# Kernel tuning notes

Hardware: AMD Instinct MI355X
Metric: run time of the kernel (lower is better)

The kernel has to match this reference:

```python
import jax, jax.numpy as jnp
import numpy as np

B, T, D, H, A, BIAS_DIM, E = 8, 1024, 1024, 16, 64, 32, 262144  # A = attention_dim_per_head


def setup_inputs() -> dict:
    key = jax.random.key(0)
    ks = jax.random.split(key, 10)
    states = jax.random.normal(ks[0], (B, T, D), dtype=jnp.float32)
    key_states = jax.random.normal(ks[1], (B, T, D), dtype=jnp.float32)
    masks = (jax.random.uniform(ks[2], (B, T, T)) < 0.1).astype(jnp.float32)
    # sparse bias edges: columns (edge_type, batch, query_idx, key_idx)
    et = jax.random.randint(ks[3], (E, 1), 0, BIAS_DIM)
    bi = jax.random.randint(ks[4], (E, 1), 0, B)
    qi = jax.random.randint(ks[5], (E, 1), 0, T)
    ki = jax.random.randint(ks[6], (E, 1), 0, T)
    attention_bias = jnp.concatenate([et, bi, qi, ki], axis=1).astype(jnp.int64)
    # parameters (xavier-like scale)
    def xav(k, shape, fan_in, fan_out):
        a = np.sqrt(6.0 / (fan_in + fan_out))
        return jax.random.uniform(k, shape, minval=-a, maxval=a, dtype=jnp.float32)
    Wq = xav(ks[7], (D, H, A), D, H * A)
    Wk = xav(jax.random.fold_in(ks[7], 1), (D, H, A), D, H * A)
    Wv = xav(jax.random.fold_in(ks[7], 2), (D, H, A), D, H * A)
    Wout = xav(ks[8], (H, A, D), H * A, D)
    bias_embs = xav(ks[9], (BIAS_DIM, A), BIAS_DIM, A)
    bias_scalar = xav(jax.random.fold_in(ks[9], 1), (A, 1), A, 1)
    return {"states": states, "key_states": key_states, "masks": masks,
            "attention_bias": attention_bias, "Wq": Wq, "Wk": Wk, "Wv": Wv,
            "Wout": Wout, "bias_embs": bias_embs, "bias_scalar": bias_scalar}


def reference(states, key_states, masks, attention_bias, Wq, Wk, Wv, Wout, bias_embs, bias_scalar):
    q = jnp.einsum('btd,dha->btha', states, Wq)
    k = jnp.einsum('btd,dha->btha', key_states, Wk)
    v = jnp.einsum('btd,dha->btha', key_states, Wv)
    alpha = jnp.einsum('bkha,bqha->bhqk', k, q)  # [B,H,Q,K]
    # sparse edge bias: embed edge types, project to scalar, scatter into [B,Q,K]
    bvals = (bias_embs[attention_bias[:, 0]] @ bias_scalar)[:, 0]  # [E]
    Bq, Hh, Q, K = alpha.shape
    bs = jnp.zeros((Bq, Q, K), dtype=alpha.dtype).at[
        attention_bias[:, 1], attention_bias[:, 2], attention_bias[:, 3]].set(bvals)
    ksum = k.sum(-1)  # [B,K,H]
    alpha = alpha + jnp.einsum('bqk,bkh->bhqk', bs, ksum)
    alpha = alpha * (1.0 / jnp.sqrt(jnp.float32(A)))
    alpha = alpha - masks[:, None, :, :] * jnp.finfo(jnp.float32).max
    alpha = jax.nn.softmax(alpha, axis=-1)
    context = jnp.einsum('bhqk,bkha->bqha', alpha, v)
    return jnp.einsum('btha,had->btd', context, Wout)
```

## Files before the change

### kernel.cpp

```cpp
#include <hip/hip_runtime.h>
#include <hip/hip_bf16.h>

#define BB 8
#define TT 1024
#define DD 1024
#define HH 16
#define AA 64
#define EE 262144

typedef unsigned short u16;
typedef unsigned int u32;
typedef short bf16x8 __attribute__((ext_vector_type(8)));
typedef float f32x4 __attribute__((ext_vector_type(4)));

__device__ __forceinline__ float bf2f(u16 u) {
    union { float f; u32 i; } c; c.i = ((u32)u) << 16; return c.f;
}
__device__ __forceinline__ u16 f2bf(float f) {
    union { float f; u32 i; } c; c.f = f;
    u32 x = c.i;
    return (u16)((x + 0x7FFFu + ((x >> 16) & 1u)) >> 16);
}
__device__ __forceinline__ u32 pack2bf(float a, float b) {
    union { __hip_bfloat162 h; u32 u; } c;
    c.h = __float22bfloat162_rn(float2{a, b});
    return c.u;
}

#define GLDS16(gp, lp)                                                        \
    __builtin_amdgcn_global_load_lds(                                         \
        (const __attribute__((address_space(1))) u32*)(const void*)(gp),      \
        (__attribute__((address_space(3))) u32*)(void*)(lp), 16, 0, 0)

#define MFMA(a, b, c) __builtin_amdgcn_mfma_f32_16x16x32_bf16((a), (b), (c), 0, 0, 0)

__global__ __launch_bounds__(256) void cvt(const float* __restrict__ src,
                                           u16* __restrict__ dst) {
    size_t i = ((size_t)blockIdx.x * 256 + threadIdx.x) * 8;
    f32x4 a = *(const f32x4*)(src + i);
    f32x4 b = *(const f32x4*)(src + i + 4);
    u32 o[4];
    o[0] = pack2bf(a[0], a[1]);
    o[1] = pack2bf(a[2], a[3]);
    o[2] = pack2bf(b[0], b[1]);
    o[3] = pack2bf(b[2], b[3]);
    *(bf16x8*)(dst + i) = *(bf16x8*)o;
}

__global__ __launch_bounds__(256) void mbinit(const float* __restrict__ masks,
                                              float* __restrict__ mb) {
    size_t i = ((size_t)blockIdx.x * 256 + threadIdx.x) * 8;
    f32x4 a = *(const f32x4*)(masks + i);
    f32x4 b = *(const f32x4*)(masks + i + 4);
    f32x4 oa, ob;
#pragma unroll
    for (int j = 0; j < 4; j++) {
        oa[j] = (a[j] != 0.f) ? -1.0e30f : 0.f;
        ob[j] = (b[j] != 0.f) ? -1.0e30f : 0.f;
    }
    *(f32x4*)(mb + i) = oa;
    *(f32x4*)(mb + i + 4) = ob;
}

__global__ __launch_bounds__(256) void scat_max(const int* __restrict__ ab,
                                                int* __restrict__ idx) {
    int e = blockIdx.x * 256 + threadIdx.x;
    const int* rec = ab + (size_t)e * 4;
    int b = rec[1], q = rec[2], k = rec[3];
    atomicMax(&idx[((((size_t)b << 10) + q) << 10) + k], e);
}

__global__ __launch_bounds__(256) void scat_res(const int* __restrict__ ab,
                                                const int* __restrict__ idx,
                                                const float* __restrict__ be,
                                                const float* __restrict__ bsc,
                                                float* __restrict__ mb) {
    __shared__ float proj[32];
    int tid = threadIdx.x;
    if (tid < 32) {
        float s = 0.f;
        for (int a = 0; a < 64; a++) s += be[tid * 64 + a] * bsc[a];
        proj[tid] = s * 0.125f;
    }
    __syncthreads();
    int e = blockIdx.x * 256 + tid;
    const int* rec = ab + (size_t)e * 4;
    int et = rec[0], b = rec[1], q = rec[2], k = rec[3];
    size_t cell = ((((size_t)b << 10) + q) << 10) + k;
    if (idx[cell] == e && mb[cell] > -1.0e29f) mb[cell] = proj[et];
}

__global__ __launch_bounds__(256) void tr_w(const float* __restrict__ s0,
                                            const float* __restrict__ s1,
                                            const float* __restrict__ s2,
                                            const float* __restrict__ s3,
                                            u16* __restrict__ dstbase) {
    __shared__ u16 t[64 * 72];
    int tid = threadIdx.x;
    int z = blockIdx.z;
    const float* src = (z == 0) ? s0 : (z == 1) ? s1 : (z == 2) ? s2 : s3;
    u16* dst = dstbase + (size_t)z * 1024 * 1024;
    int row0 = blockIdx.y * 64, col0 = blockIdx.x * 64;
    int r = tid >> 2, c0 = (tid & 3) * 16;
    const float* sp = src + (size_t)(row0 + r) * 1024 + col0 + c0;
    f32x4 f0 = *(const f32x4*)(sp);
    f32x4 f1 = *(const f32x4*)(sp + 4);
    f32x4 f2_ = *(const f32x4*)(sp + 8);
    f32x4 f3 = *(const f32x4*)(sp + 12);
#pragma unroll
    for (int j = 0; j < 4; j++) {
        t[r * 72 + c0 + j] = f2bf(f0[j]);
        t[r * 72 + c0 + 4 + j] = f2bf(f1[j]);
        t[r * 72 + c0 + 8 + j] = f2bf(f2_[j]);
        t[r * 72 + c0 + 12 + j] = f2bf(f3[j]);
    }
    __syncthreads();
    bf16x8 o0, o1;
#pragma unroll
    for (int j = 0; j < 8; j++) o0[j] = (short)t[(c0 + j) * 72 + r];
#pragma unroll
    for (int j = 0; j < 8; j++) o1[j] = (short)t[(c0 + 8 + j) * 72 + r];
    *(bf16x8*)(dst + (size_t)(col0 + r) * 1024 + row0 + c0) = o0;
    *(bf16x8*)(dst + (size_t)(col0 + r) * 1024 + row0 + c0 + 8) = o1;
}

__global__ __launch_bounds__(256) void gemm3(const u16* __restrict__ A,
                                             const u16* __restrict__ BT,
                                             void* __restrict__ C,
                                             int mode, float scale) {
    __shared__ u16 Asm[128 * 32];
    __shared__ u16 Bsm[128 * 32];
    int tid = threadIdx.x;
    int wave = tid >> 6, lane = tid & 63;
    int quad = lane >> 4, l16 = lane & 15;
    int wm = wave >> 1, wn = wave & 1;
    int mbase = blockIdx.y * 128, nbase = blockIdx.x * 128;
    f32x4 acc[4][4] = {};
    int srow = wave * 32 + (lane >> 2);
    int scol = (lane & 3) * 8;
    const u16* gA = A + (size_t)(mbase + srow) * 1024 + scol;
    const u16* gB = BT + (size_t)(nbase + srow) * 1024 + scol;
    u16* lA = Asm + wave * 32 * 32;
    u16* lB = Bsm + wave * 32 * 32;
    for (int k0 = 0; k0 < 1024; k0 += 32) {
        __syncthreads();
        GLDS16(gA + k0, lA);
        GLDS16(gA + k0 + 16 * 1024, lA + 16 * 32);
        GLDS16(gB + k0, lB);
        GLDS16(gB + k0 + 16 * 1024, lB + 16 * 32);
        __syncthreads();
        bf16x8 af[4], bfr[4];
#pragma unroll
        for (int mt = 0; mt < 4; mt++)
            af[mt] = *(const bf16x8*)&Asm[(wm * 64 + mt * 16 + l16) * 32 + quad * 8];
#pragma unroll
        for (int nt = 0; nt < 4; nt++)
            bfr[nt] = *(const bf16x8*)&Bsm[(wn * 64 + nt * 16 + l16) * 32 + quad * 8];
#pragma unroll
        for (int mt = 0; mt < 4; mt++)
#pragma unroll
            for (int nt = 0; nt < 4; nt++)
                acc[mt][nt] = MFMA(af[mt], bfr[nt], acc[mt][nt]);
    }
#pragma unroll
    for (int mt = 0; mt < 4; mt++)
#pragma unroll
        for (int nt = 0; nt < 4; nt++)
#pragma unroll
            for (int r = 0; r < 4; r++) {
                int gm = mbase + wm * 64 + mt * 16 + quad * 4 + r;
                int gn = nbase + wn * 64 + nt * 16 + l16;
                if (mode == 0) {
                    ((float*)C)[(size_t)gm * 1024 + gn] = acc[mt][nt][r];
                } else {
                    int b = gm >> 10, t = gm & 1023, h = gn >> 6, a = gn & 63;
                    ((u16*)C)[(((size_t)(b * 16 + h) * 1024) + t) * 64 + a] =
                        f2bf(acc[mt][nt][r] * scale);
                }
            }
}

__global__ __launch_bounds__(256) void tr_v(const u16* __restrict__ v,
                                            u16* __restrict__ vT) {
    __shared__ u16 t[64 * 72];
    int tid = threadIdx.x;
    int bh = blockIdx.y;
    int t0 = blockIdx.x * 64;
    int r = tid >> 2, c0 = (tid & 3) * 16;
    const u16* src = v + (size_t)bh * 1024 * 64;
    u16* dst = vT + (size_t)bh * 64 * 1024;
    bf16x8 v0 = *(const bf16x8*)(src + (size_t)(t0 + r) * 64 + c0);
    bf16x8 v1 = *(const bf16x8*)(src + (size_t)(t0 + r) * 64 + c0 + 8);
    *(bf16x8*)&t[r * 72 + c0] = v0;
    *(bf16x8*)&t[r * 72 + c0 + 8] = v1;
    __syncthreads();
    bf16x8 o0, o1;
#pragma unroll
    for (int j = 0; j < 8; j++) o0[j] = (short)t[(c0 + j) * 72 + r];
#pragma unroll
    for (int j = 0; j < 8; j++) o1[j] = (short)t[(c0 + 8 + j) * 72 + r];
    *(bf16x8*)(dst + (size_t)r * 1024 + t0 + c0) = o0;
    *(bf16x8*)(dst + (size_t)r * 1024 + t0 + c0 + 8) = o1;
}

__global__ __launch_bounds__(256) void ksumk(const u16* __restrict__ k,
                                             float* __restrict__ ks) {
    int i = blockIdx.x * 256 + threadIdx.x;
    const u16* kp = k + (size_t)i * 64;
    float s = 0.f;
#pragma unroll
    for (int c = 0; c < 64; c += 8) {
        bf16x8 v = *(const bf16x8*)(kp + c);
#pragma unroll
        for (int j = 0; j < 8; j++) s += bf2f((u16)v[j]);
    }
    ks[i] = s;
}

__global__ __launch_bounds__(256) void attn2(const u16* __restrict__ qbuf,
                                             const u16* __restrict__ kbuf,
                                             const u16* __restrict__ vT,
                                             const float* __restrict__ ksum,
                                             const float* __restrict__ mb,
                                             u16* __restrict__ ctx) {
    __shared__ u16 Ksm[64 * 72];
    __shared__ u16 Vsm[64 * 72];
    __shared__ u16 Psm[4 * 16 * 72];
    __shared__ float sksm[64];
    __shared__ float lsm[64];
    int tid = threadIdx.x;
    int wave = tid >> 6, lane = tid & 63;
    int quad = lane >> 4, l16 = lane & 15;
    int qb = blockIdx.x, h = blockIdx.y, b = blockIdx.z;
    int bh = b * 16 + h;
    const u16* qp = qbuf + (size_t)bh * 65536;
    const u16* kp = kbuf + (size_t)bh * 65536;
    const u16* vp = vT + (size_t)bh * 65536;
    const float* ksp = ksum + (size_t)bh * 1024;
    int q0 = qb * 64 + wave * 16;
    const float* mbp = mb + ((size_t)b * 1024 + (q0 + l16)) * 1024;

    bf16x8 qf0 = *(const bf16x8*)(qp + (size_t)(q0 + l16) * 64 + quad * 8);
    bf16x8 qf1 = *(const bf16x8*)(qp + (size_t)(q0 + l16) * 64 + 32 + quad * 8);

    f32x4 oacc[4] = {};
    float lsum = 0.f;
    int srow = tid >> 2, sc0 = (tid & 3) * 16;
    u16* pw = &Psm[wave * 16 * 72];

    for (int kb = 0; kb < 1024; kb += 64) {
        bf16x8 k0 = *(const bf16x8*)(kp + (size_t)(kb + srow) * 64 + sc0);
        bf16x8 k1 = *(const bf16x8*)(kp + (size_t)(kb + srow) * 64 + sc0 + 8);
        bf16x8 v0 = *(const bf16x8*)(vp + (size_t)srow * 1024 + kb + sc0);
        bf16x8 v1 = *(const bf16x8*)(vp + (size_t)srow * 1024 + kb + sc0 + 8);
        f32x4 mbv[4];
#pragma unroll
        for (int nt = 0; nt < 4; nt++)
            mbv[nt] = *(const f32x4*)(mbp + kb + nt * 16 + quad * 4);
        __syncthreads();
        *(bf16x8*)&Ksm[srow * 72 + sc0] = k0;
        *(bf16x8*)&Ksm[srow * 72 + sc0 + 8] = k1;
        *(bf16x8*)&Vsm[srow * 72 + sc0] = v0;
        *(bf16x8*)&Vsm[srow * 72 + sc0 + 8] = v1;
        if (tid < 64) sksm[tid] = ksp[kb + tid];
        __syncthreads();

        f32x4 sacc[4];
#pragma unroll
        for (int nt = 0; nt < 4; nt++) sacc[nt] = f32x4{-20.f, -20.f, -20.f, -20.f};
#pragma unroll
        for (int nt = 0; nt < 4; nt++) {
            bf16x8 kf0 = *(const bf16x8*)&Ksm[(nt * 16 + l16) * 72 + quad * 8];
            bf16x8 kf1 = *(const bf16x8*)&Ksm[(nt * 16 + l16) * 72 + 32 + quad * 8];
            sacc[nt] = MFMA(kf0, qf0, sacc[nt]);
            sacc[nt] = MFMA(kf1, qf1, sacc[nt]);
        }

#pragma unroll
        for (int nt = 0; nt < 4; nt++) {
            f32x4 k4 = *(const f32x4*)&sksm[nt * 16 + quad * 4];
            float p[4];
#pragma unroll
            for (int r = 0; r < 4; r++) {
                float e = __expf(sacc[nt][r] + mbv[nt][r] * k4[r]);
                p[r] = (mbv[nt][r] > -1.0e29f) ? e : 0.f;
                lsum += p[r];
            }
            *(u32*)&pw[l16 * 72 + nt * 16 + quad * 4] = pack2bf(p[0], p[1]);
            *(u32*)&pw[l16 * 72 + nt * 16 + quad * 4 + 2] = pack2bf(p[2], p[3]);
        }

#pragma unroll
        for (int s = 0; s < 2; s++) {
            bf16x8 pf = *(const bf16x8*)&pw[l16 * 72 + s * 32 + quad * 8];
#pragma unroll
            for (int at = 0; at < 4; at++) {
                bf16x8 vf = *(const bf16x8*)&Vsm[(at * 16 + l16) * 72 + s * 32 + quad * 8];
                oacc[at] = MFMA(pf, vf, oacc[at]);
            }
        }
    }

    lsum += __shfl_xor(lsum, 16);
    lsum += __shfl_xor(lsum, 32);
    if (lane < 16) lsm[wave * 16 + lane] = lsum;
    __syncthreads();

#pragma unroll
    for (int r = 0; r < 4; r++) {
        float linv = 1.0f / lsm[wave * 16 + quad * 4 + r];
        int q = q0 + quad * 4 + r;
#pragma unroll
        for (int at = 0; at < 4; at++) {
            ctx[(((size_t)b * 1024 + q) * 16 + h) * 64 + at * 16 + l16] =
                f2bf(oacc[at][r] * linv);
        }
    }
}

extern "C" void kernel_launch(void* const* d_in, const int* in_sizes, int n_in,
                              void* d_out, int out_size, void* d_ws, size_t ws_size,
                              hipStream_t stream) {
    const float* states = (const float*)d_in[0];
    const float* key_states = (const float*)d_in[1];
    const float* masks = (const float*)d_in[2];
    const int* abias = (const int*)d_in[3];
    const float* Wq = (const float*)d_in[4];
    const float* Wk = (const float*)d_in[5];
    const float* Wv = (const float*)d_in[6];
    const float* Wout = (const float*)d_in[7];
    const float* be = (const float*)d_in[8];
    const float* bsc = (const float*)d_in[9];

    char* ws = (char*)d_ws;
    size_t off = 0;
    auto alloc = [&](size_t n) { void* p = ws + off; off += (n + 255) & ~(size_t)255; return p; };
    u16* wT = (u16*)alloc(4ull * 1024 * 1024 * 2);
    u16* sbf = (u16*)alloc((size_t)BB * TT * DD * 2);
    u16* kbf = (u16*)alloc((size_t)BB * TT * DD * 2);
    u16* qb_ = (u16*)alloc((size_t)BB * HH * TT * AA * 2);
    u16* kb_ = (u16*)alloc((size_t)BB * HH * TT * AA * 2);
    u16* vb_ = (u16*)alloc((size_t)BB * HH * TT * AA * 2);
    u16* vT_ = (u16*)alloc((size_t)BB * HH * AA * TT * 2);
    float* ks_ = (float*)alloc((size_t)BB * HH * TT * 4);
    float* mb_ = (float*)alloc((size_t)BB * TT * TT * 4);

    u16* wqT = wT;
    u16* wkT = wT + 1048576;
    u16* wvT = wT + 2097152;
    u16* woT = wT + 3145728;
    int* idx_ = (int*)qb_;
    u16* ctx_ = vb_;

    hipMemsetAsync(idx_, 0xFF, (size_t)BB * TT * TT * 4, stream);
    mbinit<<<dim3(4096), 256, 0, stream>>>(masks, mb_);
    scat_max<<<dim3(EE / 256), 256, 0, stream>>>(abias, idx_);
    scat_res<<<dim3(EE / 256), 256, 0, stream>>>(abias, idx_, be, bsc, mb_);
    tr_w<<<dim3(16, 16, 4), 256, 0, stream>>>(Wq, Wk, Wv, Wout, wT);
    cvt<<<dim3(4096), 256, 0, stream>>>(states, sbf);
    cvt<<<dim3(4096), 256, 0, stream>>>(key_states, kbf);
    gemm3<<<dim3(8, 64), 256, 0, stream>>>(sbf, wqT, qb_, 1, 0.125f);
    gemm3<<<dim3(8, 64), 256, 0, stream>>>(kbf, wkT, kb_, 1, 1.0f);
    gemm3<<<dim3(8, 64), 256, 0, stream>>>(kbf, wvT, vb_, 1, 1.0f);
    tr_v<<<dim3(16, 128), 256, 0, stream>>>(vb_, vT_);
    ksumk<<<dim3(512), 256, 0, stream>>>(kb_, ks_);
    attn2<<<dim3(16, 16, 8), 256, 0, stream>>>(qb_, kb_, vT_, ks_, mb_, ctx_);
    gemm3<<<dim3(8, 64), 256, 0, stream>>>(ctx_, woT, d_out, 0, 1.0f);
}
```

Before: 439.9 us.

## Store mask-bias in bf16, fuse K/V GEMMs, swizzle LDS, widen attention query tile

The dense mask/bias matrix is now stored as bf16 instead of fp32, halving its write and read traffic in the attention kernel. The projection GEMM uses K-tiles of 64 with an XOR-swizzled LDS layout, and the K and V projections run as one launch over a concatenated weight. The attention kernel processes 32 queries per wave, so each K/V tile in shared memory is reused twice as much. The risks are bf16 rounding of bias values and higher register pressure in attention.

```diff
diff --git a/kernel.cpp b/kernel.cpp
--- a/kernel.cpp
+++ b/kernel.cpp
@@ -10,6 +10,7 @@
 
 typedef unsigned short u16;
 typedef unsigned int u32;
+typedef short bf16x4 __attribute__((ext_vector_type(4)));
 typedef short bf16x8 __attribute__((ext_vector_type(8)));
 typedef float f32x4 __attribute__((ext_vector_type(4)));
 
@@ -48,18 +49,18 @@
 }
 
 __global__ __launch_bounds__(256) void mbinit(const float* __restrict__ masks,
-                                              float* __restrict__ mb) {
+                                              u16* __restrict__ mb) {
     size_t i = ((size_t)blockIdx.x * 256 + threadIdx.x) * 8;
     f32x4 a = *(const f32x4*)(masks + i);
     f32x4 b = *(const f32x4*)(masks + i + 4);
-    f32x4 oa, ob;
+    const u16 M = f2bf(-1.0e30f);
+    bf16x8 o;
 #pragma unroll
     for (int j = 0; j < 4; j++) {
-        oa[j] = (a[j] != 0.f) ? -1.0e30f : 0.f;
-        ob[j] = (b[j] != 0.f) ? -1.0e30f : 0.f;
-    }
-    *(f32x4*)(mb + i) = oa;
-    *(f32x4*)(mb + i + 4) = ob;
+        o[j] = (short)((a[j] != 0.f) ? M : 0);
+        o[4 + j] = (short)((b[j] != 0.f) ? M : 0);
+    }
+    *(bf16x8*)(mb + i) = o;
 }
 
 __global__ __launch_bounds__(256) void scat_max(const int* __restrict__ ab,
@@ -74,7 +75,7 @@
                                                 const int* __restrict__ idx,
                                                 const float* __restrict__ be,
                                                 const float* __restrict__ bsc,
-                                                float* __restrict__ mb) {
+                                                u16* __restrict__ mb) {
     __shared__ float proj[32];
     int tid = threadIdx.x;
     if (tid < 32) {
@@ -87,7 +88,7 @@
     const int* rec = ab + (size_t)e * 4;
     int et = rec[0], b = rec[1], q = rec[2], k = rec[3];
     size_t cell = ((((size_t)b << 10) + q) << 10) + k;
-    if (idx[cell] == e && mb[cell] > -1.0e29f) mb[cell] = proj[et];
+    if (idx[cell] == e && bf2f(mb[cell]) > -1.0e29f) mb[cell] = f2bf(proj[et]);
 }
 
 __global__ __launch_bounds__(256) void tr_w(const float* __restrict__ s0,
@@ -124,60 +125,81 @@
     *(bf16x8*)(dst + (size_t)(col0 + r) * 1024 + row0 + c0 + 8) = o1;
 }
 
-__global__ __launch_bounds__(256) void gemm3(const u16* __restrict__ A,
+__global__ __launch_bounds__(256) void gemm4(const u16* __restrict__ A,
                                              const u16* __restrict__ BT,
-                                             void* __restrict__ C,
-                                             int mode, float scale) {
-    __shared__ u16 Asm[128 * 32];
-    __shared__ u16 Bsm[128 * 32];
+                                             void* __restrict__ C0,
+                                             void* __restrict__ C1,
+                                             void* __restrict__ C2,
+                                             int mode, float sc0) {
+    __shared__ u16 Asm[128 * 64];
+    __shared__ u16 Bsm[128 * 64];
     int tid = threadIdx.x;
     int wave = tid >> 6, lane = tid & 63;
     int quad = lane >> 4, l16 = lane & 15;
     int wm = wave >> 1, wn = wave & 1;
     int mbase = blockIdx.y * 128, nbase = blockIdx.x * 128;
     f32x4 acc[4][4] = {};
-    int srow = wave * 32 + (lane >> 2);
-    int scol = (lane & 3) * 8;
-    const u16* gA = A + (size_t)(mbase + srow) * 1024 + scol;
-    const u16* gB = BT + (size_t)(nbase + srow) * 1024 + scol;
-    u16* lA = Asm + wave * 32 * 32;
-    u16* lB = Bsm + wave * 32 * 32;
-    for (int k0 = 0; k0 < 1024; k0 += 32) {
+    int srow = wave * 32 + (lane >> 3);
+    int schunk = (lane & 7) ^ (lane >> 3);
+    const u16* gA = A + (size_t)(mbase + srow) * 1024 + schunk * 8;
+    const u16* gB = BT + (size_t)(nbase + srow) * 1024 + schunk * 8;
+    u16* lA = Asm + wave * 2048;
+    u16* lB = Bsm + wave * 2048;
+    int sx = l16 & 7;
+    for (int k0 = 0; k0 < 1024; k0 += 64) {
         __syncthreads();
-        GLDS16(gA + k0, lA);
-        GLDS16(gA + k0 + 16 * 1024, lA + 16 * 32);
-        GLDS16(gB + k0, lB);
-        GLDS16(gB + k0 + 16 * 1024, lB + 16 * 32);
+#pragma unroll
+        for (int j = 0; j < 4; j++) GLDS16(gA + k0 + j * 8192, lA + j * 512);
+#pragma unroll
+        for (int j = 0; j < 4; j++) GLDS16(gB + k0 + j * 8192, lB + j * 512);
         __syncthreads();
-        bf16x8 af[4], bfr[4];
+#pragma unroll
+        for (int kk = 0; kk < 2; kk++) {
+            bf16x8 af[4], bfr[4];
+#pragma unroll
+            for (int mt = 0; mt < 4; mt++)
+                af[mt] = *(const bf16x8*)&Asm[(wm * 64 + mt * 16 + l16) * 64 +
+                                              ((kk * 4 + quad) ^ sx) * 8];
+#pragma unroll
+            for (int nt = 0; nt < 4; nt++)
+                bfr[nt] = *(const bf16x8*)&Bsm[(wn * 64 + nt * 16 + l16) * 64 +
+                                               ((kk * 4 + quad) ^ sx) * 8];
+#pragma unroll
+            for (int mt = 0; mt < 4; mt++)
+#pragma unroll
+                for (int nt = 0; nt < 4; nt++)
+                    acc[mt][nt] = MFMA(af[mt], bfr[nt], acc[mt][nt]);
+        }
+    }
+    if (mode == 0) {
 #pragma unroll
         for (int mt = 0; mt < 4; mt++)
-            af[mt] = *(const bf16x8*)&Asm[(wm * 64 + mt * 16 + l16) * 32 + quad * 8];
-#pragma unroll
-        for (int nt = 0; nt < 4; nt++)
-            bfr[nt] = *(const bf16x8*)&Bsm[(wn * 64 + nt * 16 + l16) * 32 + quad * 8];
+#pragma unroll
+            for (int nt = 0; nt < 4; nt++)
+#pragma unroll
+                for (int r = 0; r < 4; r++) {
+                    int gm = mbase + wm * 64 + mt * 16 + quad * 4 + r;
+                    int gn = nbase + wn * 64 + nt * 16 + l16;
+                    ((float*)C0)[(size_t)gm * 1024 + gn] = acc[mt][nt][r];
+                }
+    } else {
+        int mat = nbase >> 10;
+        int nloc = nbase & 1023;
+        u16* dst = (u16*)((mat == 0) ? C0 : (mat == 1) ? C1 : C2);
+        float sc = (mat == 0) ? sc0 : 1.0f;
 #pragma unroll
         for (int mt = 0; mt < 4; mt++)
 #pragma unroll
             for (int nt = 0; nt < 4; nt++)
-                acc[mt][nt] = MFMA(af[mt], bfr[nt], acc[mt][nt]);
-    }
-#pragma unroll
-    for (int mt = 0; mt < 4; mt++)
-#pragma unroll
-        for (int nt = 0; nt < 4; nt++)
-#pragma unroll
-            for (int r = 0; r < 4; r++) {
-                int gm = mbase + wm * 64 + mt * 16 + quad * 4 + r;
-                int gn = nbase + wn * 64 + nt * 16 + l16;
-                if (mode == 0) {
-                    ((float*)C)[(size_t)gm * 1024 + gn] = acc[mt][nt][r];
-                } else {
-                    int b = gm >> 10, t = gm & 1023, h = gn >> 6, a = gn & 63;
-                    ((u16*)C)[(((size_t)(b * 16 + h) * 1024) + t) * 64 + a] =
-                        f2bf(acc[mt][nt][r] * scale);
+#pragma unroll
+                for (int r = 0; r < 4; r++) {
+                    int gm = mbase + wm * 64 + mt * 16 + quad * 4 + r;
+                    int gnl = nloc + wn * 64 + nt * 16 + l16;
+                    int b = gm >> 10, t = gm & 1023, h = gnl >> 6, a = gnl & 63;
+                    dst[(((size_t)(b * 16 + h) * 1024) + t) * 64 + a] =
+                        f2bf(acc[mt][nt][r] * sc);
                 }
-            }
+    }
 }
 
 __global__ __launch_bounds__(256) void tr_v(const u16* __restrict__ v,
@@ -217,17 +239,17 @@
     ks[i] = s;
 }
 
-__global__ __launch_bounds__(256) void attn2(const u16* __restrict__ qbuf,
+__global__ __launch_bounds__(256) void attn3(const u16* __restrict__ qbuf,
                                              const u16* __restrict__ kbuf,
                                              const u16* __restrict__ vT,
                                              const float* __restrict__ ksum,
-                                             const float* __restrict__ mb,
+                                             const u16* __restrict__ mb,
                                              u16* __restrict__ ctx) {
     __shared__ u16 Ksm[64 * 72];
     __shared__ u16 Vsm[64 * 72];
     __shared__ u16 Psm[4 * 16 * 72];
     __shared__ float sksm[64];
-    __shared__ float lsm[64];
+    __shared__ float lsm[128];
     int tid = threadIdx.x;
     int wave = tid >> 6, lane = tid & 63;
     int quad = lane >> 4, l16 = lane & 15;
@@ -237,14 +259,19 @@
     const u16* kp = kbuf + (size_t)bh * 65536;
     const u16* vp = vT + (size_t)bh * 65536;
     const float* ksp = ksum + (size_t)bh * 1024;
-    int q0 = qb * 64 + wave * 16;
-    const float* mbp = mb + ((size_t)b * 1024 + (q0 + l16)) * 1024;
-
-    bf16x8 qf0 = *(const bf16x8*)(qp + (size_t)(q0 + l16) * 64 + quad * 8);
-    bf16x8 qf1 = *(const bf16x8*)(qp + (size_t)(q0 + l16) * 64 + 32 + quad * 8);
-
-    f32x4 oacc[4] = {};
-    float lsum = 0.f;
+    int q0w = qb * 128 + wave * 32;
+    const u16* mbp[2];
+    bf16x8 qf[2][2];
+#pragma unroll
+    for (int s = 0; s < 2; s++) {
+        int qs = q0w + s * 16;
+        mbp[s] = mb + ((size_t)b * 1024 + qs + l16) * 1024;
+        qf[s][0] = *(const bf16x8*)(qp + (size_t)(qs + l16) * 64 + quad * 8);
+        qf[s][1] = *(const bf16x8*)(qp + (size_t)(qs + l16) * 64 + 32 + quad * 8);
+    }
+
+    f32x4 oacc[2][4] = {};
+    float lsum[2] = {0.f, 0.f};
     int srow = tid >> 2, sc0 = (tid & 3) * 16;
     u16* pw = &Psm[wave * 16 * 72];
 
@@ -253,10 +280,12 @@
         bf16x8 k1 = *(const bf16x8*)(kp + (size_t)(kb + srow) * 64 + sc0 + 8);
         bf16x8 v0 = *(const bf16x8*)(vp + (size_t)srow * 1024 + kb + sc0);
         bf16x8 v1 = *(const bf16x8*)(vp + (size_t)srow * 1024 + kb + sc0 + 8);
-        f32x4 mbv[4];
-#pragma unroll
-        for (int nt = 0; nt < 4; nt++)
-            mbv[nt] = *(const f32x4*)(mbp + kb + nt * 16 + quad * 4);
+        bf16x4 mraw[2][4];
+#pragma unroll
+        for (int s = 0; s < 2; s++)
+#pragma unroll
+            for (int nt = 0; nt < 4; nt++)
+                mraw[s][nt] = *(const bf16x4*)(mbp[s] + kb + nt * 16 + quad * 4);
         __syncthreads();
         *(bf16x8*)&Ksm[srow * 72 + sc0] = k0;
         *(bf16x8*)&Ksm[srow * 72 + sc0 + 8] = k1;
@@ -265,57 +294,64 @@
         if (tid < 64) sksm[tid] = ksp[kb + tid];
         __syncthreads();
 
-        f32x4 sacc[4];
-#pragma unroll
-        for (int nt = 0; nt < 4; nt++) sacc[nt] = f32x4{-20.f, -20.f, -20.f, -20.f};
-#pragma unroll
-        for (int nt = 0; nt < 4; nt++) {
-            bf16x8 kf0 = *(const bf16x8*)&Ksm[(nt * 16 + l16) * 72 + quad * 8];
-            bf16x8 kf1 = *(const bf16x8*)&Ksm[(nt * 16 + l16) * 72 + 32 + quad * 8];
-            sacc[nt] = MFMA(kf0, qf0, sacc[nt]);
-            sacc[nt] = MFMA(kf1, qf1, sacc[nt]);
-        }
-
-#pragma unroll
-        for (int nt = 0; nt < 4; nt++) {
-            f32x4 k4 = *(const f32x4*)&sksm[nt * 16 + quad * 4];
-            float p[4];
-#pragma unroll
-            for (int r = 0; r < 4; r++) {
-                float e = __expf(sacc[nt][r] + mbv[nt][r] * k4[r]);
-                p[r] = (mbv[nt][r] > -1.0e29f) ? e : 0.f;
-                lsum += p[r];
+#pragma unroll
+        for (int s = 0; s < 2; s++) {
+            f32x4 sacc[4];
+#pragma unroll
+            for (int nt = 0; nt < 4; nt++) sacc[nt] = f32x4{-20.f, -20.f, -20.f, -20.f};
+#pragma unroll
+            for (int nt = 0; nt < 4; nt++) {
+                bf16x8 kf0 = *(const bf16x8*)&Ksm[(nt * 16 + l16) * 72 + quad * 8];
+                bf16x8 kf1 = *(const bf16x8*)&Ksm[(nt * 16 + l16) * 72 + 32 + quad * 8];
+                sacc[nt] = MFMA(kf0, qf[s][0], sacc[nt]);
+                sacc[nt] = MFMA(kf1, qf[s][1], sacc[nt]);
             }
-            *(u32*)&pw[l16 * 72 + nt * 16 + quad * 4] = pack2bf(p[0], p[1]);
-            *(u32*)&pw[l16 * 72 + nt * 16 + quad * 4 + 2] = pack2bf(p[2], p[3]);
-        }
-
-#pragma unroll
-        for (int s = 0; s < 2; s++) {
-            bf16x8 pf = *(const bf16x8*)&pw[l16 * 72 + s * 32 + quad * 8];
-#pragma unroll
-            for (int at = 0; at < 4; at++) {
-                bf16x8 vf = *(const bf16x8*)&Vsm[(at * 16 + l16) * 72 + s * 32 + quad * 8];
-                oacc[at] = MFMA(pf, vf, oacc[at]);
+#pragma unroll
+            for (int nt = 0; nt < 4; nt++) {
+                f32x4 k4 = *(const f32x4*)&sksm[nt * 16 + quad * 4];
+                float p[4];
+#pragma unroll
+                for (int r = 0; r < 4; r++) {
+                    float f = bf2f((u16)mraw[s][nt][r]);
+                    float e = __expf(sacc[nt][r] + f * k4[r]);
+                    p[r] = (f > -1.0e29f) ? e : 0.f;
+                    lsum[s] += p[r];
+                }
+                *(u32*)&pw[l16 * 72 + nt * 16 + quad * 4] = pack2bf(p[0], p[1]);
+                *(u32*)&pw[l16 * 72 + nt * 16 + quad * 4 + 2] = pack2bf(p[2], p[3]);
+            }
+#pragma unroll
+            for (int hs = 0; hs < 2; hs++) {
+                bf16x8 pf = *(const bf16x8*)&pw[l16 * 72 + hs * 32 + quad * 8];
+#pragma unroll
+                for (int at = 0; at < 4; at++) {
+                    bf16x8 vf = *(const bf16x8*)&Vsm[(at * 16 + l16) * 72 + hs * 32 + quad * 8];
+                    oacc[s][at] = MFMA(pf, vf, oacc[s][at]);
+                }
             }
         }
     }
 
-    lsum += __shfl_xor(lsum, 16);
-    lsum += __shfl_xor(lsum, 32);
-    if (lane < 16) lsm[wave * 16 + lane] = lsum;
+#pragma unroll
+    for (int s = 0; s < 2; s++) {
+        lsum[s] += __shfl_xor(lsum[s], 16);
+        lsum[s] += __shfl_xor(lsum[s], 32);
+        if (lane < 16) lsm[wave * 32 + s * 16 + lane] = lsum[s];
+    }
     __syncthreads();
 
 #pragma unroll
-    for (int r = 0; r < 4; r++) {
-        float linv = 1.0f / lsm[wave * 16 + quad * 4 + r];
-        int q = q0 + quad * 4 + r;
-#pragma unroll
-        for (int at = 0; at < 4; at++) {
-            ctx[(((size_t)b * 1024 + q) * 16 + h) * 64 + at * 16 + l16] =
-                f2bf(oacc[at][r] * linv);
+    for (int s = 0; s < 2; s++)
+#pragma unroll
+        for (int r = 0; r < 4; r++) {
+            float linv = 1.0f / lsm[wave * 32 + s * 16 + quad * 4 + r];
+            int q = q0w + s * 16 + quad * 4 + r;
+#pragma unroll
+            for (int at = 0; at < 4; at++) {
+                ctx[(((size_t)b * 1024 + q) * 16 + h) * 64 + at * 16 + l16] =
+                    f2bf(oacc[s][at][r] * linv);
+            }
         }
-    }
 }
 
 extern "C" void kernel_launch(void* const* d_in, const int* in_sizes, int n_in,
@@ -343,11 +379,10 @@
     u16* vb_ = (u16*)alloc((size_t)BB * HH * TT * AA * 2);
     u16* vT_ = (u16*)alloc((size_t)BB * HH * AA * TT * 2);
     float* ks_ = (float*)alloc((size_t)BB * HH * TT * 4);
-    float* mb_ = (float*)alloc((size_t)BB * TT * TT * 4);
+    u16* mb_ = (u16*)alloc((size_t)BB * TT * TT * 2);
 
     u16* wqT = wT;
-    u16* wkT = wT + 1048576;
-    u16* wvT = wT + 2097152;
+    u16* wkvT = wT + 1048576;
     u16* woT = wT + 3145728;
     int* idx_ = (int*)qb_;
     u16* ctx_ = vb_;
@@ -359,11 +394,10 @@
     tr_w<<<dim3(16, 16, 4), 256, 0, stream>>>(Wq, Wk, Wv, Wout, wT);
     cvt<<<dim3(4096), 256, 0, stream>>>(states, sbf);
     cvt<<<dim3(4096), 256, 0, stream>>>(key_states, kbf);
-    gemm3<<<dim3(8, 64), 256, 0, stream>>>(sbf, wqT, qb_, 1, 0.125f);
-    gemm3<<<dim3(8, 64), 256, 0, stream>>>(kbf, wkT, kb_, 1, 1.0f);
-    gemm3<<<dim3(8, 64), 256, 0, stream>>>(kbf, wvT, vb_, 1, 1.0f);
+    gemm4<<<dim3(8, 64), 256, 0, stream>>>(sbf, wqT, qb_, nullptr, nullptr, 1, 0.125f);
+    gemm4<<<dim3(16, 64), 256, 0, stream>>>(kbf, wkvT, kb_, vb_, nullptr, 1, 1.0f);
     tr_v<<<dim3(16, 128), 256, 0, stream>>>(vb_, vT_);
     ksumk<<<dim3(512), 256, 0, stream>>>(kb_, ks_);
-    attn2<<<dim3(16, 16, 8), 256, 0, stream>>>(qb_, kb_, vT_, ks_, mb_, ctx_);
-    gemm3<<<dim3(8, 64), 256, 0, stream>>>(ctx_, woT, d_out, 0, 1.0f);
-}
+    attn3<<<dim3(8, 16, 8), 256, 0, stream>>>(qb_, kb_, vT_, ks_, mb_, ctx_);
+    gemm4<<<dim3(8, 64), 256, 0, stream>>>(ctx_, woT, d_out, nullptr, nullptr, 0, 1.0f);
+}
```

After: 410.9 us. -6.6%, faster.
